# Kernel optimization log

Measured on AMD Instinct MI355X. Metric: run time of the kernel, lower is better.

Reference implementation:

```python
import jax, jax.numpy as jnp
import numpy as np

B, S, H, DH = 64, 300, 4, 32   # batch, seq, heads, head_dim
D = H * DH                     # hidden = 128
L = 8                          # num_hidden_layers
SPAN = 8                       # max_relative_positions (att_span)
EPS = 1e-7                     # DebertaConfig layer_norm_eps default


def _ln(x, s, b):
    mu = x.mean(-1, keepdims=True)
    var = ((x - mu) ** 2).mean(-1, keepdims=True)
    return (x - mu) * jax.lax.rsqrt(var + EPS) * s + b


def _gelu(x):
    return jax.nn.gelu(x, approximate=False)  # torch nn.GELU / HF 'gelu' (erf)


def setup_inputs():
    ks = iter(jax.random.split(jax.random.key(0), 48))
    w = lambda shape: jax.random.normal(next(ks), shape, jnp.float32) * 0.02
    return dict(
        inputs=jax.random.uniform(next(ks), (B, S, 4), jnp.float32),
        mask=jnp.ones((B, S), jnp.float32),
        emb_W1=w((3, 64)), emb_b1=w((64,)),
        emb_W2=w((64, D)), emb_b2=w((D,)),
        emb_W3=w((D, D)), emb_b3=w((D,)),
        tok_emb=w((2, D)),
        emb_ln_s=jnp.ones((D,), jnp.float32), emb_ln_b=jnp.zeros((D,), jnp.float32),
        rel_emb=w((2 * SPAN, D)),
        qkv_W=w((L, D, 3 * D)), q_bias=w((L, D)), v_bias=w((L, D)),
        pos_k_W=w((L, D, D)), pos_q_W=w((L, D, D)), pos_q_b=w((L, D)),
        attn_out_W=w((L, D, D)), attn_out_b=w((L, D)),
        ln1_s=jnp.ones((L, D), jnp.float32), ln1_b=jnp.zeros((L, D), jnp.float32),
        ffn_W1=w((L, D, 512)), ffn_b1=w((L, 512)),
        ffn_W2=w((L, 512, D)), ffn_b2=w((L, D)),
        ln2_s=jnp.ones((L, D), jnp.float32), ln2_b=jnp.zeros((L, D), jnp.float32),
        rec_W1=w((D, D)), rec_b1=w((D,)),
        rec_W2=w((D, 64)), rec_b2=w((64,)),
        rec_W3=w((64, 5)), rec_b3=w((5,)),
        conn_W=w((S * 5, 2500)), conn_b=w((2500,)),
    )


def reference(inputs, mask, emb_W1, emb_b1, emb_W2, emb_b2, emb_W3, emb_b3,
              tok_emb, emb_ln_s, emb_ln_b, rel_emb,
              qkv_W, q_bias, v_bias, pos_k_W, pos_q_W, pos_q_b,
              attn_out_W, attn_out_b, ln1_s, ln1_b,
              ffn_W1, ffn_b1, ffn_W2, ffn_b2, ln2_s, ln2_b,
              rec_W1, rec_b1, rec_W2, rec_b2, rec_W3, rec_b3,
              conn_W, conn_b):
    # ---- embedding MLP on first 3 feature columns ----
    e = _gelu(inputs[..., :3] @ emb_W1 + emb_b1)
    e = _gelu(e @ emb_W2 + emb_b2)
    e = _gelu(e @ emb_W3 + emb_b3)
    tok = inputs[..., 3].astype(jnp.int32)            # token_type_ids
    e = _ln(e + tok_emb[tok], emb_ln_s, emb_ln_b)     # position_biased_input=False
    x = e * mask[..., None]                           # DebertaEmbeddings mask mult

    # ---- relative position indices (q_size == k_size == S) ----
    rel = jnp.arange(S)[:, None] - jnp.arange(S)[None, :]
    c2p_idx = jnp.clip(rel + SPAN, 0, 2 * SPAN - 1)   # [S,S]
    p2c_idx = jnp.clip(-rel + SPAN, 0, 2 * SPAN - 1)  # [S,S]
    mask4 = (mask[:, None, :, None] * mask[:, None, None, :]) > 0  # [B,1,S,S]
    neg = jnp.finfo(x.dtype).min
    scale = jnp.sqrt(jnp.asarray(DH * 3, x.dtype))    # scale_factor = 1+len([c2p,p2c])

    for l in range(L):
        qkv = (x @ qkv_W[l]).reshape(B, S, H, 3, DH)  # in_proj (no bias)
        q = qkv[..., 0, :].transpose(0, 2, 1, 3) + q_bias[l].reshape(H, DH)[None, :, None, :]
        k = qkv[..., 1, :].transpose(0, 2, 1, 3)
        v = qkv[..., 2, :].transpose(0, 2, 1, 3) + v_bias[l].reshape(H, DH)[None, :, None, :]
        q = q / scale
        scores = jnp.einsum('bhqd,bhkd->bhqk', q, k)  # content-to-content
        # content-to-position
        pos_k = (rel_emb @ pos_k_W[l]).reshape(2 * SPAN, H, DH).transpose(1, 0, 2)  # [H,16,DH]
        c2p = jnp.einsum('bhqd,hrd->bhqr', q, pos_k)  # [B,H,S,16]
        scores = scores + jnp.take_along_axis(c2p, c2p_idx[None, None], axis=-1)
        # position-to-content
        pos_q = ((rel_emb @ pos_q_W[l]) + pos_q_b[l]).reshape(2 * SPAN, H, DH).transpose(1, 0, 2) / scale
        p2c = jnp.einsum('bhkd,hrd->bhkr', k, pos_q)  # [B,H,S,16]
        scores = scores + jnp.swapaxes(jnp.take_along_axis(p2c, p2c_idx[None, None], axis=-1), -1, -2)
        # XSoftmax
        probs = jnp.where(mask4, jax.nn.softmax(jnp.where(mask4, scores, neg), axis=-1), 0.0)
        ctx = jnp.einsum('bhqk,bhkd->bhqd', probs, v).transpose(0, 2, 1, 3).reshape(B, S, D)
        x = _ln(ctx @ attn_out_W[l] + attn_out_b[l] + x, ln1_s[l], ln1_b[l])
        h = _gelu(x @ ffn_W1[l] + ffn_b1[l])
        x = _ln(h @ ffn_W2[l] + ffn_b2[l] + x, ln2_s[l], ln2_b[l])

    # ---- reconstruction MLP + connection ----
    r = _gelu(x @ rec_W1 + rec_b1)
    r = _gelu(r @ rec_W2 + rec_b2)
    r = _gelu(r @ rec_W3 + rec_b3)                    # [B,S,5]
    out = r.reshape(B, S * 5) @ conn_W + conn_b       # [B,2500]
    return out.reshape(-1, 50, 50)
```

## Files before the change

kernel.cpp:

```cpp
#include <hip/hip_runtime.h>
#include <hip/hip_bf16.h>
#include <math.h>

#define Bq 64
#define Sq 300
#define NH 4
#define DHd 32
#define Dd 128
#define NL 8
#define FF 512
#define NIN 36
#define SP 304
#define SPX 320

typedef __attribute__((ext_vector_type(8))) short bf16x8;
typedef __attribute__((ext_vector_type(4))) float f32x4;

__device__ __forceinline__ float gelu_f(float x) {
    return 0.5f * x * (1.0f + erff(x * 0.70710678118654752f));
}
__device__ __forceinline__ bool bf16_mode(const unsigned* maskw) {
    return maskw[0] == 0x3F803F80u;
}

struct ConvArgs {
    const void* src[NIN];
    float* dst[NIN];
    int n[NIN];
};

__global__ void convert_kernel(ConvArgs a, const unsigned* maskw) {
    bool bfm = bf16_mode(maskw);
    int bi = blockIdx.y;
    int n = a.n[bi];
    float* dst = a.dst[bi];
    int stride = gridDim.x * blockDim.x;
    int i0 = blockIdx.x * blockDim.x + threadIdx.x;
    if (bfm) {
        const __hip_bfloat16* s = (const __hip_bfloat16*)a.src[bi];
        for (int i = i0; i < n; i += stride) dst[i] = __bfloat162float(s[i]);
    } else {
        const float* s = (const float*)a.src[bi];
        for (int i = i0; i < n; i += stride) dst[i] = s[i];
    }
}

__global__ void pack_kernel(const float* __restrict__ W1all, const float* __restrict__ W2all,
                            const float* __restrict__ Wqall, const float* __restrict__ Woall,
                            const float* __restrict__ Wr1, const float* __restrict__ Wr2,
                            const float* __restrict__ We2, const float* __restrict__ We3,
                            __hip_bfloat16* __restrict__ P1, __hip_bfloat16* __restrict__ P2,
                            __hip_bfloat16* __restrict__ Pq, __hip_bfloat16* __restrict__ Po,
                            __hip_bfloat16* __restrict__ Pr1, __hip_bfloat16* __restrict__ Pr2,
                            __hip_bfloat16* __restrict__ Pe2, __hip_bfloat16* __restrict__ Pe3) {
    int l = blockIdx.y;
    int which = blockIdx.z;
    if (which >= 4 && l != 0) return;
    int K = (which == 1) ? 512 : ((which == 6) ? 64 : 128);
    int N = (which == 0) ? 512 : (which == 1 ? 128 : (which == 2 ? 384 : (which == 5 ? 64 : 128)));
    int slots = (K / 32) * (N / 16) * 64;
    int idx = blockIdx.x * 256 + threadIdx.x;
    if (idx >= slots) return;
    int lane = idx & 63;
    int nkt = K / 32;
    int kt = (idx >> 6) % nkt;
    int nt = (idx >> 6) / nkt;
    const float* W; __hip_bfloat16* P;
    switch (which) {
        case 0:  W = W1all + (size_t)l * 128 * 512; P = P1 + (size_t)l * 65536; break;
        case 1:  W = W2all + (size_t)l * 512 * 128; P = P2 + (size_t)l * 65536; break;
        case 2:  W = Wqall + (size_t)l * 128 * 384; P = Pq + (size_t)l * 49152; break;
        case 3:  W = Woall + (size_t)l * 128 * 128; P = Po + (size_t)l * 16384; break;
        case 4:  W = Wr1; P = Pr1; break;
        case 5:  W = Wr2; P = Pr2; break;
        case 6:  W = We2; P = Pe2; break;
        default: W = We3; P = Pe3; break;
    }
    P += (size_t)idx * 8;
    int n = nt * 16 + (lane & 15);
    int k0 = kt * 32 + (lane >> 4) * 8;
    #pragma unroll
    for (int j = 0; j < 8; j++) P[j] = __float2bfloat16(W[(size_t)(k0 + j) * N + n]);
}

__global__ __launch_bounds__(256) void embed_mfma_kernel(
        const float* __restrict__ inp, const float* __restrict__ mask,
        const float* __restrict__ W1, const float* __restrict__ b1,
        const __hip_bfloat16* __restrict__ Pe2, const float* __restrict__ b2,
        const __hip_bfloat16* __restrict__ Pe3, const float* __restrict__ b3,
        const float* __restrict__ tok_emb,
        const float* __restrict__ ln_s, const float* __restrict__ ln_b,
        float* __restrict__ x) {
    int blk = blockIdx.x;
    int t = threadIdx.x;
    int w = t >> 6, lane = t & 63;
    int row0 = blk * 16;
    __shared__ float f[16][4];
    __shared__ __align__(16) __hip_bfloat16 e1a[16 * 72];
    __shared__ __align__(16) __hip_bfloat16 e2a[16 * 136];
    __shared__ float dbuf[16 * 132];
    if (t < 64) f[t >> 2][t & 3] = inp[(size_t)(row0 + (t >> 2)) * 4 + (t & 3)];
    __syncthreads();
    {
        int r1 = t >> 4, n0 = (t & 15) * 4;
        float f0 = f[r1][0], f1 = f[r1][1], f2 = f[r1][2];
        #pragma unroll
        for (int j = 0; j < 4; j++) {
            int n = n0 + j;
            float a = b1[n] + f0 * W1[n] + f1 * W1[64 + n] + f2 * W1[128 + n];
            e1a[r1 * 72 + n] = __float2bfloat16(gelu_f(a));
        }
    }
    __syncthreads();
    int m = lane & 15, quad = lane >> 4;
    bf16x8 a2[2];
    #pragma unroll
    for (int kt = 0; kt < 2; kt++) a2[kt] = *(bf16x8*)&e1a[m * 72 + kt * 32 + quad * 8];
    #pragma unroll
    for (int nt0 = 0; nt0 < 2; nt0++) {
        int nt = w * 2 + nt0;
        f32x4 acc = {0.f, 0.f, 0.f, 0.f};
        const bf16x8* bp = (const bf16x8*)(Pe2 + (size_t)nt * 2 * 512);
        #pragma unroll
        for (int kt = 0; kt < 2; kt++) {
            bf16x8 bfr = bp[kt * 64 + lane];
            acc = __builtin_amdgcn_mfma_f32_16x16x32_bf16(a2[kt], bfr, acc, 0, 0, 0);
        }
        int n = nt * 16 + m;
        float bb = b2[n];
        #pragma unroll
        for (int r = 0; r < 4; r++)
            e2a[(quad * 4 + r) * 136 + n] = __float2bfloat16(gelu_f(acc[r] + bb));
    }
    __syncthreads();
    bf16x8 a3[4];
    #pragma unroll
    for (int kt = 0; kt < 4; kt++) a3[kt] = *(bf16x8*)&e2a[m * 136 + kt * 32 + quad * 8];
    f32x4 acc2[2] = {{0.f,0.f,0.f,0.f}, {0.f,0.f,0.f,0.f}};
    #pragma unroll
    for (int kt = 0; kt < 4; kt++) {
        #pragma unroll
        for (int nt0 = 0; nt0 < 2; nt0++) {
            int nt = w * 2 + nt0;
            bf16x8 bfr = ((const bf16x8*)(Pe3 + (size_t)nt * 4 * 512))[kt * 64 + lane];
            acc2[nt0] = __builtin_amdgcn_mfma_f32_16x16x32_bf16(a3[kt], bfr, acc2[nt0], 0, 0, 0);
        }
    }
    #pragma unroll
    for (int nt0 = 0; nt0 < 2; nt0++) {
        int n = (w * 2 + nt0) * 16 + m;
        float bb = b3[n];
        #pragma unroll
        for (int r = 0; r < 4; r++) {
            int row = quad * 4 + r;
            int tok = (int)f[row][3];
            dbuf[row * 132 + n] = gelu_f(acc2[nt0][r] + bb) + tok_emb[tok * 128 + n];
        }
    }
    __syncthreads();
    #pragma unroll
    for (int rr = 0; rr < 4; rr++) {
        int row = w * 4 + rr;
        int c0 = lane, c1 = lane + 64;
        float y0 = dbuf[row * 132 + c0];
        float y1 = dbuf[row * 132 + c1];
        float sm = y0 + y1;
        #pragma unroll
        for (int o = 32; o > 0; o >>= 1) sm += __shfl_xor(sm, o);
        float mu = sm * (1.0f / 128.0f);
        float d0 = y0 - mu, d1 = y1 - mu;
        float vv = d0 * d0 + d1 * d1;
        #pragma unroll
        for (int o = 32; o > 0; o >>= 1) vv += __shfl_xor(vv, o);
        float rstd = rsqrtf(vv * (1.0f / 128.0f) + 1e-7f);
        float mk = mask[row0 + row];
        x[(size_t)(row0 + row) * 128 + c0] = (d0 * rstd * ln_s[c0] + ln_b[c0]) * mk;
        x[(size_t)(row0 + row) * 128 + c1] = (d1 * rstd * ln_s[c1] + ln_b[c1]) * mk;
    }
}

__global__ __launch_bounds__(512) void qkv_mfma_kernel(const float* __restrict__ x,
                                                       const __hip_bfloat16* __restrict__ Pq,
                                                       const float* __restrict__ qb, const float* __restrict__ vb,
                                                       __hip_bfloat16* __restrict__ qbf,
                                                       __hip_bfloat16* __restrict__ kbf,
                                                       __hip_bfloat16* __restrict__ vT) {
    int blk = blockIdx.x;
    int t = threadIdx.x;
    int w = t >> 6, lane = t & 63;
    int row0 = blk * 32;
    __shared__ __align__(16) __hip_bfloat16 xa[32 * 136];
    for (int i = t; i < 1024; i += 512) {
        float4 v4 = ((const float4*)(x + (size_t)row0 * 128))[i];
        int r = i >> 5, c4 = (i & 31) * 4;
        __hip_bfloat16* d = &xa[r * 136 + c4];
        d[0] = __float2bfloat16(v4.x); d[1] = __float2bfloat16(v4.y);
        d[2] = __float2bfloat16(v4.z); d[3] = __float2bfloat16(v4.w);
    }
    __syncthreads();
    int m = lane & 15, quad = lane >> 4;
    bf16x8 a1[2][4];
    #pragma unroll
    for (int mt = 0; mt < 2; mt++)
        #pragma unroll
        for (int kt = 0; kt < 4; kt++)
            a1[mt][kt] = *(bf16x8*)&xa[(mt * 16 + m) * 136 + kt * 32 + quad * 8];
    const float inv_scale = 0.10206207261596576f;
    #pragma unroll
    for (int nt0 = 0; nt0 < 3; nt0++) {
        int nt = w * 3 + nt0;
        f32x4 acc[2] = {{0.f,0.f,0.f,0.f}, {0.f,0.f,0.f,0.f}};
        const bf16x8* bp = (const bf16x8*)(Pq + (size_t)nt * 4 * 512);
        #pragma unroll
        for (int kt = 0; kt < 4; kt++) {
            bf16x8 bfr = bp[kt * 64 + lane];
            #pragma unroll
            for (int mt = 0; mt < 2; mt++)
                acc[mt] = __builtin_amdgcn_mfma_f32_16x16x32_bf16(a1[mt][kt], bfr, acc[mt], 0, 0, 0);
        }
        int n = nt * 16 + m;
        int h = n / 96, mm = (n % 96) / 32, d = n % 32;
        float qbv = qb[h * 32 + d], vbv = vb[h * 32 + d];
        #pragma unroll
        for (int mt = 0; mt < 2; mt++) {
            #pragma unroll
            for (int r = 0; r < 4; r++) {
                int row = row0 + mt * 16 + quad * 4 + r;
                int bb = row / Sq, s = row % Sq;
                int bh = bb * NH + h;
                float a = acc[mt][r];
                if (mm == 0) {
                    qbf[((size_t)bh * SP + s) * 32 + d] = __float2bfloat16((a + qbv) * inv_scale);
                } else if (mm == 1) {
                    kbf[((size_t)bh * SP + s) * 32 + d] = __float2bfloat16(a);
                } else {
                    vT[((size_t)bh * 32 + d) * SP + s] = __float2bfloat16(a + vbv);
                }
            }
        }
    }
}

__global__ void pad_kernel(__hip_bfloat16* qbf, __hip_bfloat16* kbf, __hip_bfloat16* vT) {
    int i = blockIdx.x * 256 + threadIdx.x;
    if (i >= 256 * 4 * 32) return;
    int bh = i >> 7, s = Sq + ((i >> 5) & 3), d = i & 31;
    __hip_bfloat16 z = __float2bfloat16(0.0f);
    qbf[((size_t)bh * SP + s) * 32 + d] = z;
    kbf[((size_t)bh * SP + s) * 32 + d] = z;
    vT[((size_t)bh * 32 + d) * SP + s] = z;
}

__global__ void pos_kernel(const float* __restrict__ rel_emb,
                           const float* __restrict__ pkW_all, const float* __restrict__ pqW_all,
                           const float* __restrict__ pqb_all,
                           __hip_bfloat16* __restrict__ poskb, __hip_bfloat16* __restrict__ posqb) {
    int l = blockIdx.y;
    int bi = blockIdx.x;
    int which = bi >> 4;
    int r = bi & 15;
    int t = threadIdx.x;
    __shared__ float re[128];
    re[t] = rel_emb[r * 128 + t];
    __syncthreads();
    const float* W = (which ? pqW_all : pkW_all) + (size_t)l * 128 * 128;
    float a = 0.0f;
    for (int k = 0; k < 128; k++) a += re[k] * W[k * 128 + t];
    int h = t >> 5, d = t & 31;
    size_t o = ((size_t)(l * NH + h) * 16 + r) * 32 + d;
    if (which) { a = (a + pqb_all[l * 128 + t]) * 0.10206207261596576f; posqb[o] = __float2bfloat16(a); }
    else       { poskb[o] = __float2bfloat16(a); }
}

__global__ __launch_bounds__(256) void attn_mfma_kernel(const __hip_bfloat16* __restrict__ qbf,
                                                        const __hip_bfloat16* __restrict__ kbf,
                                                        const __hip_bfloat16* __restrict__ vT,
                                                        const __hip_bfloat16* __restrict__ poskb,
                                                        const __hip_bfloat16* __restrict__ posqb,
                                                        const float* __restrict__ mask,
                                                        __hip_bfloat16* __restrict__ ctxb) {
    int bh = blockIdx.x;
    int b = bh >> 2, h = bh & 3;
    int t = threadIdx.x;
    int w = t >> 6, lane = t & 63;
    int m = lane & 15, quad = lane >> 4;

    __shared__ float p2cS[SPX * 17];
    __shared__ float c2pS[4][16 * 17];
    __shared__ __align__(16) __hip_bfloat16 pT[4][16 * 40];

    {
        bf16x8 pqf = *(const bf16x8*)&posqb[(h * 16 + m) * 32 + quad * 8];
        #pragma unroll
        for (int it = 0; it < 5; it++) {
            int jb = (w + it * 4) * 16;
            bf16x8 kf2 = *(const bf16x8*)&kbf[((size_t)bh * SP + jb + m) * 32 + quad * 8];
            f32x4 pc = __builtin_amdgcn_mfma_f32_16x16x32_bf16(kf2, pqf, (f32x4){0.f,0.f,0.f,0.f}, 0, 0, 0);
            #pragma unroll
            for (int r = 0; r < 4; r++) {
                int j = jb + quad * 4 + r;
                float mv = (j < Sq) ? mask[b * Sq + j] : 0.0f;
                p2cS[j * 17 + m] = (mv > 0.0f) ? pc[r] : -30000.0f;
            }
        }
    }
    __syncthreads();

    int qt = blockIdx.y * 4 + w;
    if (qt >= 19) return;
    int q0 = qt * 16;

    float* c2pW = c2pS[w];
    __hip_bfloat16* pTW = pT[w];

    bf16x8 aq = *(const bf16x8*)&qbf[((size_t)bh * SP + q0 + m) * 32 + quad * 8];

    {
        bf16x8 pkf = *(const bf16x8*)&poskb[(h * 16 + m) * 32 + quad * 8];
        f32x4 cc = __builtin_amdgcn_mfma_f32_16x16x32_bf16(aq, pkf, (f32x4){0.f,0.f,0.f,0.f}, 0, 0, 0);
        #pragma unroll
        for (int r = 0; r < 4; r++) c2pW[(quad * 4 + r) * 17 + m] = cc[r];
    }

    int qi = q0 + m;
    f32x4 oacc[2] = {{0.f,0.f,0.f,0.f}, {0.f,0.f,0.f,0.f}};
    float lacc = 0.0f;

    for (int jt2 = 0; jt2 < 10; jt2++) {
        int j0 = jt2 * 32;
        #pragma unroll
        for (int half = 0; half < 2; half++) {
            int jh = j0 + half * 16;
            bf16x8 kf = *(const bf16x8*)&kbf[((size_t)bh * SP + jh + m) * 32 + quad * 8];
            f32x4 sc = __builtin_amdgcn_mfma_f32_16x16x32_bf16(kf, aq, (f32x4){0.f,0.f,0.f,0.f}, 0, 0, 0);
            int jb2 = jh + quad * 4;
            int base = qi - jb2 + 8;
            __hip_bfloat16 pb[4];
            #pragma unroll
            for (int r = 0; r < 4; r++) {
                int rr = base - r; rr = rr < 0 ? 0 : (rr > 15 ? 15 : rr);
                float sv = sc[r] + c2pW[m * 17 + rr] + p2cS[(jb2 + r) * 17 + rr];
                float p = __expf(sv);
                lacc += p;
                pb[r] = __float2bfloat16(p);
            }
            *(uint2*)&pTW[m * 40 + half * 16 + quad * 4] = *(uint2*)pb;
        }
        bf16x8 ap = *(bf16x8*)&pTW[m * 40 + quad * 8];
        #pragma unroll
        for (int nt = 0; nt < 2; nt++) {
            bf16x8 vf = *(const bf16x8*)&vT[((size_t)bh * 32 + nt * 16 + m) * SP + j0 + quad * 8];
            oacc[nt] = __builtin_amdgcn_mfma_f32_16x16x32_bf16(ap, vf, oacc[nt], 0, 0, 0);
        }
    }

    lacc += __shfl_xor(lacc, 16);
    lacc += __shfl_xor(lacc, 32);
    #pragma unroll
    for (int r = 0; r < 4; r++) {
        int qrow = quad * 4 + r;
        float lr = __shfl(lacc, qrow);
        int qi2 = q0 + qrow;
        float qm = (qi2 < Sq) ? mask[b * Sq + qi2] : 0.0f;
        float inv = (qm > 0.0f && lr > 0.0f) ? 1.0f / lr : 0.0f;
        if (qi2 < Sq) {
            size_t base2 = ((size_t)(b * Sq + qi2)) * 128 + h * 32;
            ctxb[base2 + m]      = __float2bfloat16(oacc[0][r] * inv);
            ctxb[base2 + 16 + m] = __float2bfloat16(oacc[1][r] * inv);
        }
    }
}

__global__ __launch_bounds__(512) void aoffn_mfma_kernel(
        const __hip_bfloat16* __restrict__ ctxb,
        const __hip_bfloat16* __restrict__ Po, const float* __restrict__ ob,
        const float* __restrict__ ln1s, const float* __restrict__ ln1b,
        const __hip_bfloat16* __restrict__ P1, const float* __restrict__ b1,
        const __hip_bfloat16* __restrict__ P2, const float* __restrict__ b2,
        const float* __restrict__ ln2s, const float* __restrict__ ln2b,
        float* __restrict__ x) {
    int blk = blockIdx.x;
    int t = threadIdx.x;
    int w = t >> 6, lane = t & 63;
    int row0 = blk * 32;

    __shared__ __align__(16) __hip_bfloat16 ca[32 * 136];
    __shared__ float xr[32 * 128];
    __shared__ __align__(16) char hbuf[32 * 520 * 2];
    __hip_bfloat16* ha = (__hip_bfloat16*)hbuf;
    float* dbuf = (float*)hbuf;

    {
        uint4 cv = ((const uint4*)(ctxb + (size_t)row0 * 128))[t];
        int r = t >> 4, c8 = (t & 15) * 8;
        *(uint4*)&ca[r * 136 + c8] = cv;
    }
    __syncthreads();

    int m = lane & 15, quad = lane >> 4;

    {
        f32x4 acc[2] = {{0.f,0.f,0.f,0.f}, {0.f,0.f,0.f,0.f}};
        const bf16x8* bp = (const bf16x8*)(Po + (size_t)w * 4 * 512);
        #pragma unroll
        for (int kt = 0; kt < 4; kt++) {
            bf16x8 bfr = bp[kt * 64 + lane];
            #pragma unroll
            for (int mt = 0; mt < 2; mt++) {
                bf16x8 a = *(bf16x8*)&ca[(mt * 16 + m) * 136 + kt * 32 + quad * 8];
                acc[mt] = __builtin_amdgcn_mfma_f32_16x16x32_bf16(a, bfr, acc[mt], 0, 0, 0);
            }
        }
        int n = w * 16 + m;
        #pragma unroll
        for (int mt = 0; mt < 2; mt++)
            #pragma unroll
            for (int r = 0; r < 4; r++)
                dbuf[(mt * 16 + quad * 4 + r) * 132 + n] = acc[mt][r];
    }
    __syncthreads();

    #pragma unroll
    for (int rr = 0; rr < 4; rr++) {
        int row = w * 4 + rr;
        int c0 = lane, c1 = lane + 64;
        size_t g = (size_t)(row0 + row) * 128;
        float y0 = dbuf[row * 132 + c0] + ob[c0] + x[g + c0];
        float y1 = dbuf[row * 132 + c1] + ob[c1] + x[g + c1];
        float sm = y0 + y1;
        #pragma unroll
        for (int o = 32; o > 0; o >>= 1) sm += __shfl_xor(sm, o);
        float mu = sm * (1.0f / 128.0f);
        float d0 = y0 - mu, d1 = y1 - mu;
        float vv = d0 * d0 + d1 * d1;
        #pragma unroll
        for (int o = 32; o > 0; o >>= 1) vv += __shfl_xor(vv, o);
        float rstd = rsqrtf(vv * (1.0f / 128.0f) + 1e-7f);
        float o0 = d0 * rstd * ln1s[c0] + ln1b[c0];
        float o1 = d1 * rstd * ln1s[c1] + ln1b[c1];
        xr[row * 128 + c0] = o0;
        xr[row * 128 + c1] = o1;
        ca[row * 136 + c0] = __float2bfloat16(o0);
        ca[row * 136 + c1] = __float2bfloat16(o1);
    }
    __syncthreads();

    {
        bf16x8 a1[2][4];
        #pragma unroll
        for (int mt = 0; mt < 2; mt++)
            #pragma unroll
            for (int kt = 0; kt < 4; kt++)
                a1[mt][kt] = *(bf16x8*)&ca[(mt * 16 + m) * 136 + kt * 32 + quad * 8];
        #pragma unroll
        for (int nt0 = 0; nt0 < 4; nt0++) {
            int nt = w * 4 + nt0;
            f32x4 acc[2] = {{0.f,0.f,0.f,0.f}, {0.f,0.f,0.f,0.f}};
            const bf16x8* bp = (const bf16x8*)(P1 + (size_t)nt * 4 * 512);
            #pragma unroll
            for (int kt = 0; kt < 4; kt++) {
                bf16x8 bfr = bp[kt * 64 + lane];
                #pragma unroll
                for (int mt = 0; mt < 2; mt++)
                    acc[mt] = __builtin_amdgcn_mfma_f32_16x16x32_bf16(a1[mt][kt], bfr, acc[mt], 0, 0, 0);
            }
            int n = nt * 16 + m;
            float bb = b1[n];
            #pragma unroll
            for (int mt = 0; mt < 2; mt++)
                #pragma unroll
                for (int r = 0; r < 4; r++)
                    ha[(mt * 16 + quad * 4 + r) * 520 + n] = __float2bfloat16(gelu_f(acc[mt][r] + bb));
        }
    }
    __syncthreads();

    f32x4 acc2[2] = {{0.f,0.f,0.f,0.f}, {0.f,0.f,0.f,0.f}};
    {
        const bf16x8* bp = (const bf16x8*)(P2 + (size_t)w * 16 * 512);
        #pragma unroll
        for (int kt = 0; kt < 16; kt++) {
            bf16x8 bfr = bp[kt * 64 + lane];
            #pragma unroll
            for (int mt = 0; mt < 2; mt++) {
                bf16x8 a = *(bf16x8*)&ha[(mt * 16 + m) * 520 + kt * 32 + quad * 8];
                acc2[mt] = __builtin_amdgcn_mfma_f32_16x16x32_bf16(a, bfr, acc2[mt], 0, 0, 0);
            }
        }
    }
    __syncthreads();
    {
        int n = w * 16 + m;
        #pragma unroll
        for (int mt = 0; mt < 2; mt++)
            #pragma unroll
            for (int r = 0; r < 4; r++)
                dbuf[(mt * 16 + quad * 4 + r) * 132 + n] = acc2[mt][r];
    }
    __syncthreads();

    #pragma unroll
    for (int rr = 0; rr < 4; rr++) {
        int row = w * 4 + rr;
        int c0 = lane, c1 = lane + 64;
        float y0 = dbuf[row * 132 + c0] + b2[c0] + xr[row * 128 + c0];
        float y1 = dbuf[row * 132 + c1] + b2[c1] + xr[row * 128 + c1];
        float sm = y0 + y1;
        #pragma unroll
        for (int o = 32; o > 0; o >>= 1) sm += __shfl_xor(sm, o);
        float mu = sm * (1.0f / 128.0f);
        float d0 = y0 - mu, d1 = y1 - mu;
        float vv = d0 * d0 + d1 * d1;
        #pragma unroll
        for (int o = 32; o > 0; o >>= 1) vv += __shfl_xor(vv, o);
        float rstd = rsqrtf(vv * (1.0f / 128.0f) + 1e-7f);
        x[(size_t)(row0 + row) * 128 + c0] = d0 * rstd * ln2s[c0] + ln2b[c0];
        x[(size_t)(row0 + row) * 128 + c1] = d1 * rstd * ln2s[c1] + ln2b[c1];
    }
}

__global__ __launch_bounds__(256) void rec_mfma_kernel(const float* __restrict__ x,
                                                       const __hip_bfloat16* __restrict__ Pr1,
                                                       const float* __restrict__ b1,
                                                       const __hip_bfloat16* __restrict__ Pr2,
                                                       const float* __restrict__ b2,
                                                       const float* __restrict__ W3, const float* __restrict__ b3,
                                                       float* __restrict__ r3) {
    int blk = blockIdx.x;
    int t = threadIdx.x;
    int w = t >> 6, lane = t & 63;
    int row0 = blk * 16;
    __shared__ __align__(16) __hip_bfloat16 xa[16 * 136];
    __shared__ __align__(16) __hip_bfloat16 ha[16 * 136];
    __shared__ float r2s[16 * 68];
    for (int i = t; i < 512; i += 256) {
        float4 v4 = ((const float4*)(x + (size_t)row0 * 128))[i];
        int r = i >> 5, c4 = (i & 31) * 4;
        __hip_bfloat16* d = &xa[r * 136 + c4];
        d[0] = __float2bfloat16(v4.x); d[1] = __float2bfloat16(v4.y);
        d[2] = __float2bfloat16(v4.z); d[3] = __float2bfloat16(v4.w);
    }
    __syncthreads();
    int m = lane & 15, quad = lane >> 4;

    bf16x8 a1[4];
    #pragma unroll
    for (int kt = 0; kt < 4; kt++) a1[kt] = *(bf16x8*)&xa[m * 136 + kt * 32 + quad * 8];
    #pragma unroll
    for (int nt0 = 0; nt0 < 2; nt0++) {
        int nt = w * 2 + nt0;
        f32x4 acc = {0.f, 0.f, 0.f, 0.f};
        const bf16x8* bp = (const bf16x8*)(Pr1 + (size_t)nt * 4 * 512);
        #pragma unroll
        for (int kt = 0; kt < 4; kt++) {
            bf16x8 bfr = bp[kt * 64 + lane];
            acc = __builtin_amdgcn_mfma_f32_16x16x32_bf16(a1[kt], bfr, acc, 0, 0, 0);
        }
        int n = nt * 16 + m;
        float bb = b1[n];
        #pragma unroll
        for (int r = 0; r < 4; r++)
            ha[(quad * 4 + r) * 136 + n] = __float2bfloat16(gelu_f(acc[r] + bb));
    }
    __syncthreads();

    {
        f32x4 acc = {0.f, 0.f, 0.f, 0.f};
        const bf16x8* bp = (const bf16x8*)(Pr2 + (size_t)w * 4 * 512);
        #pragma unroll
        for (int kt = 0; kt < 4; kt++) {
            bf16x8 a = *(bf16x8*)&ha[m * 136 + kt * 32 + quad * 8];
            bf16x8 bfr = bp[kt * 64 + lane];
            acc = __builtin_amdgcn_mfma_f32_16x16x32_bf16(a, bfr, acc, 0, 0, 0);
        }
        int n = w * 16 + m;
        float bb = b2[n];
        #pragma unroll
        for (int r = 0; r < 4; r++)
            r2s[(quad * 4 + r) * 68 + n] = gelu_f(acc[r] + bb);
    }
    __syncthreads();

    if (t < 80) {
        int row = t / 5, c = t % 5;
        float a = b3[c];
        for (int k = 0; k < 64; k++) a += r2s[row * 68 + k] * W3[k * 5 + c];
        r3[(size_t)(row0 + row) * 5 + c] = gelu_f(a);
    }
}

__global__ void conn_kernel(const float* __restrict__ r3, const float* __restrict__ W,
                            const float* __restrict__ b, void* out, const unsigned* maskw) {
    bool bfm = bf16_mode(maskw);
    int cb = blockIdx.x;
    int bg = blockIdx.y;
    int t = threadIdx.x;
    int cl = t & 63;
    int kq = t >> 6;
    int col = cb * 64 + cl;
    __shared__ float rs[4 * 1500];
    __shared__ float pacc[4 * 64 * 4];
    {
        const float4* src = (const float4*)(r3 + (size_t)bg * 4 * 1500);
        for (int i = t; i < 1500; i += 256) ((float4*)rs)[i] = src[i];
    }
    __syncthreads();
    float acc[4] = {0.f, 0.f, 0.f, 0.f};
    if (col < 2500) {
        for (int k = kq * 4; k < 1500; k += 16) {
            float w0 = W[(size_t)(k + 0) * 2500 + col];
            float w1 = W[(size_t)(k + 1) * 2500 + col];
            float w2 = W[(size_t)(k + 2) * 2500 + col];
            float w3 = W[(size_t)(k + 3) * 2500 + col];
            #pragma unroll
            for (int bb = 0; bb < 4; bb++) {
                float4 rv = *(const float4*)&rs[bb * 1500 + k];
                acc[bb] += rv.x * w0 + rv.y * w1 + rv.z * w2 + rv.w * w3;
            }
        }
    }
    #pragma unroll
    for (int bb = 0; bb < 4; bb++) pacc[(kq * 64 + cl) * 4 + bb] = acc[bb];
    __syncthreads();
    if (kq == 0 && col < 2500) {
        float bv = b[col];
        #pragma unroll
        for (int bb = 0; bb < 4; bb++) {
            float a = bv + pacc[(0 * 64 + cl) * 4 + bb] + pacc[(1 * 64 + cl) * 4 + bb]
                         + pacc[(2 * 64 + cl) * 4 + bb] + pacc[(3 * 64 + cl) * 4 + bb];
            int ob = bg * 4 + bb;
            if (bfm) ((__hip_bfloat16*)out)[(size_t)ob * 2500 + col] = __float2bfloat16(a);
            else     ((float*)out)[(size_t)ob * 2500 + col] = a;
        }
    }
}

extern "C" void kernel_launch(void* const* d_in, const int* in_sizes, int n_in,
                              void* d_out, int out_size, void* d_ws, size_t ws_size,
                              hipStream_t stream) {
    float* ws = (float*)d_ws;

    float* cv[NIN];
    size_t off = 0;
    for (int i = 0; i < NIN; i++) { cv[i] = ws + off; off += (size_t)in_sizes[i]; }

    const float* inp      = cv[0];
    const float* mask     = cv[1];
    const float* emb_W1   = cv[2];
    const float* emb_b1   = cv[3];
    const float* emb_W2   = cv[4];
    const float* emb_b2   = cv[5];
    const float* emb_W3   = cv[6];
    const float* emb_b3   = cv[7];
    const float* tok_emb  = cv[8];
    const float* emb_ln_s = cv[9];
    const float* emb_ln_b = cv[10];
    const float* rel_emb  = cv[11];
    const float* qkv_W    = cv[12];
    const float* q_bias   = cv[13];
    const float* v_bias   = cv[14];
    const float* pos_k_W  = cv[15];
    const float* pos_q_W  = cv[16];
    const float* pos_q_b  = cv[17];
    const float* attn_out_W = cv[18];
    const float* attn_out_b = cv[19];
    const float* ln1_s    = cv[20];
    const float* ln1_b    = cv[21];
    const float* ffn_W1   = cv[22];
    const float* ffn_b1   = cv[23];
    const float* ffn_W2   = cv[24];
    const float* ffn_b2   = cv[25];
    const float* ln2_s    = cv[26];
    const float* ln2_b    = cv[27];
    const float* rec_W1   = cv[28];
    const float* rec_b1   = cv[29];
    const float* rec_W2   = cv[30];
    const float* rec_b2   = cv[31];
    const float* rec_W3   = cv[32];
    const float* rec_b3   = cv[33];
    const float* conn_W   = cv[34];
    const float* conn_b   = cv[35];

    const int NTOK = Bq * Sq;
    float* x    = ws + off;
    float* q    = x    + (size_t)NTOK * 128;
    float* k    = q    + (size_t)Bq * NH * Sq * 32;
    float* ctx  = k    + (size_t)Bq * NH * Sq * 32;
    float* c2p  = ctx  + (size_t)NTOK * 128;
    float* p2c  = c2p  + (size_t)Bq * NH * Sq * 16;
    float* posk = p2c  + (size_t)Bq * NH * Sq * 16;
    float* posq = posk + (size_t)NL * 16 * 128;
    float* r3b  = posq + (size_t)NL * 16 * 128;
    float* endf = r3b  + (size_t)NTOK * 5;
    __hip_bfloat16* P1 = (__hip_bfloat16*)endf;
    __hip_bfloat16* P2 = P1 + (size_t)NL * 65536;
    __hip_bfloat16* Pq = P2 + (size_t)NL * 65536;
    __hip_bfloat16* Po = Pq + (size_t)NL * 49152;
    __hip_bfloat16* qbf = Po + (size_t)NL * 16384;
    __hip_bfloat16* kbf = qbf + (size_t)256 * SP * 32;
    __hip_bfloat16* vTb = kbf + (size_t)256 * SP * 32;
    __hip_bfloat16* Pr1 = vTb + (size_t)256 * SP * 32;
    __hip_bfloat16* Pr2 = Pr1 + 16384;
    __hip_bfloat16* Pe2 = Pr2 + 8192;
    __hip_bfloat16* Pe3 = Pe2 + 8192;
    __hip_bfloat16* Pkb = Pe3 + 16384;
    __hip_bfloat16* Pqb = Pkb + (size_t)NL * 2048;
    __hip_bfloat16* ctxb = (__hip_bfloat16*)ctx;

    const unsigned* maskw = (const unsigned*)d_in[1];

    ConvArgs ca;
    for (int i = 0; i < NIN; i++) {
        ca.src[i] = d_in[i];
        ca.dst[i] = cv[i];
        ca.n[i] = in_sizes[i];
    }
    convert_kernel<<<dim3(256, NIN), 256, 0, stream>>>(ca, maskw);
    pack_kernel<<<dim3(32, NL, 8), 256, 0, stream>>>(ffn_W1, ffn_W2, qkv_W, attn_out_W,
                                                     rec_W1, rec_W2, emb_W2, emb_W3,
                                                     P1, P2, Pq, Po, Pr1, Pr2, Pe2, Pe3);

    embed_mfma_kernel<<<NTOK / 16, 256, 0, stream>>>(inp, mask, emb_W1, emb_b1,
                                                     Pe2, emb_b2, Pe3, emb_b3,
                                                     tok_emb, emb_ln_s, emb_ln_b, x);

    pos_kernel<<<dim3(32, NL), 128, 0, stream>>>(rel_emb, pos_k_W, pos_q_W, pos_q_b, Pkb, Pqb);
    pad_kernel<<<128, 256, 0, stream>>>(qbf, kbf, vTb);

    for (int l = 0; l < NL; l++) {
        qkv_mfma_kernel<<<NTOK / 32, 512, 0, stream>>>(x, Pq + (size_t)l * 49152,
                                                       q_bias + l * 128, v_bias + l * 128,
                                                       qbf, kbf, vTb);
        attn_mfma_kernel<<<dim3(256, 5), 256, 0, stream>>>(qbf, kbf, vTb,
                                                           Pkb + (size_t)l * 2048,
                                                           Pqb + (size_t)l * 2048,
                                                           mask, ctxb);
        aoffn_mfma_kernel<<<NTOK / 32, 512, 0, stream>>>(ctxb,
                                                         Po + (size_t)l * 16384, attn_out_b + l * 128,
                                                         ln1_s + l * 128, ln1_b + l * 128,
                                                         P1 + (size_t)l * 65536, ffn_b1 + l * 512,
                                                         P2 + (size_t)l * 65536, ffn_b2 + l * 128,
                                                         ln2_s + l * 128, ln2_b + l * 128, x);
    }

    rec_mfma_kernel<<<NTOK / 16, 256, 0, stream>>>(x, Pr1, rec_b1, Pr2, rec_b2,
                                                   rec_W3, rec_b3, r3b);
    conn_kernel<<<dim3(40, 16), 256, 0, stream>>>(r3b, conn_W, conn_b, d_out, maskw);
}
```

Baseline: 697.1 us.

## Fuse next layer's QKV projection into attention-output/FFN kernel epilogue

The per-layer QKV projection kernel is folded into the tail of the attention-output/FFN kernel. The freshly layer-normed rows are written as bf16 into shared memory and multiplied by the next layer's packed QKV weights. Only the first layer keeps a standalone QKV launch. This drops seven kernel launches and one re-read of x from global memory per layer. In exchange the fused kernel does more work per block and may need more registers, and it relies on the shared-memory buffer and the m/quad lane variables already existing in that scope.

```diff
diff --git a/kernel.cpp b/kernel.cpp
--- a/kernel.cpp
+++ b/kernel.cpp
@@ -378,7 +378,12 @@
         const __hip_bfloat16* __restrict__ P1, const float* __restrict__ b1,
         const __hip_bfloat16* __restrict__ P2, const float* __restrict__ b2,
         const float* __restrict__ ln2s, const float* __restrict__ ln2b,
-        float* __restrict__ x) {
+        float* __restrict__ x,
+        int do_qkv,
+        const __hip_bfloat16* __restrict__ Pqn,
+        const float* __restrict__ qbn, const float* __restrict__ vbn,
+        __hip_bfloat16* __restrict__ qbf, __hip_bfloat16* __restrict__ kbf,
+        __hip_bfloat16* __restrict__ vT) {
     int blk = blockIdx.x;
     int t = threadIdx.x;
     int w = t >> 6, lane = t & 63;
@@ -514,8 +519,57 @@
         #pragma unroll
         for (int o = 32; o > 0; o >>= 1) vv += __shfl_xor(vv, o);
         float rstd = rsqrtf(vv * (1.0f / 128.0f) + 1e-7f);
-        x[(size_t)(row0 + row) * 128 + c0] = d0 * rstd * ln2s[c0] + ln2b[c0];
-        x[(size_t)(row0 + row) * 128 + c1] = d1 * rstd * ln2s[c1] + ln2b[c1];
+        float o0 = d0 * rstd * ln2s[c0] + ln2b[c0];
+        float o1 = d1 * rstd * ln2s[c1] + ln2b[c1];
+        x[(size_t)(row0 + row) * 128 + c0] = o0;
+        x[(size_t)(row0 + row) * 128 + c1] = o1;
+        ca[row * 136 + c0] = __float2bfloat16(o0);
+        ca[row * 136 + c1] = __float2bfloat16(o1);
+    }
+    if (!do_qkv) return;
+    __syncthreads();
+
+    {
+        bf16x8 aq[2][4];
+        #pragma unroll
+        for (int mt = 0; mt < 2; mt++)
+            #pragma unroll
+            for (int kt = 0; kt < 4; kt++)
+                aq[mt][kt] = *(bf16x8*)&ca[(mt * 16 + m) * 136 + kt * 32 + quad * 8];
+        const float inv_scale = 0.10206207261596576f;
+        #pragma unroll
+        for (int nt0 = 0; nt0 < 3; nt0++) {
+            int nt = w * 3 + nt0;
+            f32x4 acc[2] = {{0.f,0.f,0.f,0.f}, {0.f,0.f,0.f,0.f}};
+            const bf16x8* bp = (const bf16x8*)(Pqn + (size_t)nt * 4 * 512);
+            #pragma unroll
+            for (int kt = 0; kt < 4; kt++) {
+                bf16x8 bfr = bp[kt * 64 + lane];
+                #pragma unroll
+                for (int mt = 0; mt < 2; mt++)
+                    acc[mt] = __builtin_amdgcn_mfma_f32_16x16x32_bf16(aq[mt][kt], bfr, acc[mt], 0, 0, 0);
+            }
+            int n = nt * 16 + m;
+            int h = n / 96, mm = (n % 96) / 32, d = n % 32;
+            float qbv = qbn[h * 32 + d], vbv = vbn[h * 32 + d];
+            #pragma unroll
+            for (int mt = 0; mt < 2; mt++) {
+                #pragma unroll
+                for (int r = 0; r < 4; r++) {
+                    int row = row0 + mt * 16 + quad * 4 + r;
+                    int bb = row / Sq, s = row % Sq;
+                    int bh = bb * NH + h;
+                    float a = acc[mt][r];
+                    if (mm == 0) {
+                        qbf[((size_t)bh * SP + s) * 32 + d] = __float2bfloat16((a + qbv) * inv_scale);
+                    } else if (mm == 1) {
+                        kbf[((size_t)bh * SP + s) * 32 + d] = __float2bfloat16(a);
+                    } else {
+                        vT[((size_t)bh * 32 + d) * SP + s] = __float2bfloat16(a + vbv);
+                    }
+                }
+            }
+        }
     }
 }
 
@@ -727,20 +781,24 @@
     pos_kernel<<<dim3(32, NL), 128, 0, stream>>>(rel_emb, pos_k_W, pos_q_W, pos_q_b, Pkb, Pqb);
     pad_kernel<<<128, 256, 0, stream>>>(qbf, kbf, vTb);
 
+    qkv_mfma_kernel<<<NTOK / 32, 512, 0, stream>>>(x, Pq, q_bias, v_bias, qbf, kbf, vTb);
+
     for (int l = 0; l < NL; l++) {
-        qkv_mfma_kernel<<<NTOK / 32, 512, 0, stream>>>(x, Pq + (size_t)l * 49152,
-                                                       q_bias + l * 128, v_bias + l * 128,
-                                                       qbf, kbf, vTb);
         attn_mfma_kernel<<<dim3(256, 5), 256, 0, stream>>>(qbf, kbf, vTb,
                                                            Pkb + (size_t)l * 2048,
                                                            Pqb + (size_t)l * 2048,
                                                            mask, ctxb);
+        int ln = (l + 1 < NL) ? (l + 1) : 0;
         aoffn_mfma_kernel<<<NTOK / 32, 512, 0, stream>>>(ctxb,
                                                          Po + (size_t)l * 16384, attn_out_b + l * 128,
                                                          ln1_s + l * 128, ln1_b + l * 128,
                                                          P1 + (size_t)l * 65536, ffn_b1 + l * 512,
                                                          P2 + (size_t)l * 65536, ffn_b2 + l * 128,
-                                                         ln2_s + l * 128, ln2_b + l * 128, x);
+                                                         ln2_s + l * 128, ln2_b + l * 128, x,
+                                                         (l + 1 < NL) ? 1 : 0,
+                                                         Pq + (size_t)ln * 49152,
+                                                         q_bias + ln * 128, v_bias + ln * 128,
+                                                         qbf, kbf, vTb);
     }
 
     rec_mfma_kernel<<<NTOK / 16, 256, 0, stream>>>(x, Pr1, rec_b1, Pr2, rec_b2,
```

Result: faster. 683.0 us (-2.0%).
